# Kernel tuning notes

Hardware: AMD Instinct MI355X
Metric: run time of the kernel (lower is better)

The kernel has to match this reference:

```python
import jax, jax.numpy as jnp
import numpy as np

D_MODEL = 1024
NUM_HEADS = 16
HEAD_DIM = D_MODEL // NUM_HEADS

def setup_inputs() -> dict:
    key = jax.random.key(0)
    ks = jax.random.split(key, 9)
    B, L = 2, 2048
    s = 1.0 / np.sqrt(D_MODEL)
    return {
        "x":  jax.random.normal(ks[0], (B, L, D_MODEL), dtype=jnp.float32),
        "Wq": jax.random.uniform(ks[1], (D_MODEL, D_MODEL), jnp.float32, -s, s),
        "bq": jax.random.uniform(ks[2], (D_MODEL,), jnp.float32, -s, s),
        "Wk": jax.random.uniform(ks[3], (D_MODEL, D_MODEL), jnp.float32, -s, s),
        "bk": jax.random.uniform(ks[4], (D_MODEL,), jnp.float32, -s, s),
        "Wv": jax.random.uniform(ks[5], (D_MODEL, D_MODEL), jnp.float32, -s, s),
        "bv": jax.random.uniform(ks[6], (D_MODEL,), jnp.float32, -s, s),
        "Wo": jax.random.uniform(ks[7], (D_MODEL, D_MODEL), jnp.float32, -s, s),
        "bo": jax.random.uniform(ks[8], (D_MODEL,), jnp.float32, -s, s),
    }

def _split_heads(t):
    B, L, _ = t.shape
    return t.reshape(B, L, NUM_HEADS, HEAD_DIM).transpose(0, 2, 1, 3)  # [B,H,L,Dh]

def reference(x, Wq, bq, Wk, bk, Wv, bv, Wo, bo):
    # Linear projections (torch Linear: y = x @ W.T + b)
    Q = _split_heads(x @ Wq.T + bq)
    K = _split_heads(x @ Wk.T + bk)
    V = _split_heads(x @ Wv.T + bv)
    scale = 1.0 / jnp.sqrt(jnp.asarray(HEAD_DIM, dtype=x.dtype))
    scores = jnp.einsum('bhqd,bhkd->bhqk', Q, K) * scale  # [B,H,L,L]
    attn_weights = jax.nn.softmax(scores, axis=-1)
    ctx = jnp.einsum('bhqk,bhkd->bhqd', attn_weights, V)  # [B,H,L,Dh]
    B, H, L, Dh = ctx.shape
    ctx = ctx.transpose(0, 2, 1, 3).reshape(B, L, H * Dh)
    out = ctx @ Wo.T + bo  # dropout p=0.0 -> identity
    return (out, attn_weights)
```

## Files before the change

### kernel.cpp

```cpp
#include <hip/hip_runtime.h>

typedef unsigned short u16;
typedef __bf16 bf16x8 __attribute__((ext_vector_type(8)));
typedef float f32x4 __attribute__((ext_vector_type(4)));

#define WSTR 72
#define TSZ (64 * WSTR)

__device__ __forceinline__ u16 f2bf(float f) {
    union { float f; unsigned int u; } v; v.f = f;
    unsigned int u = v.u;
    u += 0x7fffu + ((u >> 16) & 1u);
    return (u16)(u >> 16);
}

__device__ __forceinline__ u16 cvt_bf(float f) {
    __bf16 h = (__bf16)f;
    union { __bf16 h; u16 u; } v; v.h = h; return v.u;
}

__device__ __forceinline__ void gload16(const u16* g, u16* l) {
    __builtin_amdgcn_global_load_lds((const __attribute__((address_space(1))) unsigned int*)(const void*)g,
                                     (__attribute__((address_space(3))) unsigned int*)(void*)l, 16, 0, 0);
}

#define MFMA16(A, B, C) __builtin_amdgcn_mfma_f32_16x16x32_bf16(A, B, C, 0, 0, 0)

__global__ __launch_bounds__(256) void k_cvtX(const float* __restrict__ src, u16* __restrict__ dst) {
    const size_t i = ((size_t)blockIdx.x * 256 + threadIdx.x) * 8;
    float4 v0 = *(const float4*)(src + i);
    float4 v1 = *(const float4*)(src + i + 4);
    u16 o[8];
    o[0] = f2bf(v0.x); o[1] = f2bf(v0.y); o[2] = f2bf(v0.z); o[3] = f2bf(v0.w);
    o[4] = f2bf(v1.x); o[5] = f2bf(v1.y); o[6] = f2bf(v1.z); o[7] = f2bf(v1.w);
    *(uint4*)(dst + i) = *(const uint4*)o;
}

__global__ __launch_bounds__(256) void k_cvtW(const float* __restrict__ w0, const float* __restrict__ w1,
                                              const float* __restrict__ w2, const float* __restrict__ w3,
                                              u16* __restrict__ dst) {
    const int z = blockIdx.z;
    const float* src = z == 0 ? w0 : z == 1 ? w1 : z == 2 ? w2 : w3;
    const size_t i = ((size_t)blockIdx.x * 256 + threadIdx.x) * 8;
    float4 v0 = *(const float4*)(src + i);
    float4 v1 = *(const float4*)(src + i + 4);
    u16 o[8];
    o[0] = f2bf(v0.x); o[1] = f2bf(v0.y); o[2] = f2bf(v0.z); o[3] = f2bf(v0.w);
    o[4] = f2bf(v1.x); o[5] = f2bf(v1.y); o[6] = f2bf(v1.z); o[7] = f2bf(v1.w);
    *(uint4*)(dst + (size_t)z * 1048576 + i) = *(const uint4*)o;
}

__global__ __launch_bounds__(256) void k_qkv(const u16* __restrict__ Xb, const u16* __restrict__ Wb,
                                             const float* __restrict__ bq, const float* __restrict__ bk,
                                             const float* __restrict__ bv,
                                             u16* __restrict__ Q, u16* __restrict__ Kd, u16* __restrict__ Vtmp) {
    __shared__ __align__(16) u16 lA[128 * 32];
    __shared__ __align__(16) u16 lB[128 * 32];
    const int t = threadIdx.x;
    const int n0 = blockIdx.x * 128;
    const int m0 = blockIdx.y * 128;
    const int lane = t & 63, wave = t >> 6;
    const int wm = (wave >> 1) * 64, wn = (wave & 1) * 64;
    const int quad = lane >> 4, m16 = lane & 15;
    const int r4 = t >> 2, c8 = (t & 3) * 8;
    f32x4 acc[4][4] = {};
    for (int k0 = 0; k0 < 1024; k0 += 32) {
        gload16(Xb + (size_t)(m0 + r4) * 1024 + k0 + c8,       &lA[t * 8]);
        gload16(Xb + (size_t)(m0 + 64 + r4) * 1024 + k0 + c8,  &lA[2048 + t * 8]);
        gload16(Wb + (size_t)(n0 + r4) * 1024 + k0 + c8,       &lB[t * 8]);
        gload16(Wb + (size_t)(n0 + 64 + r4) * 1024 + k0 + c8,  &lB[2048 + t * 8]);
        __syncthreads();
        bf16x8 af[4], bfr[4];
#pragma unroll
        for (int i = 0; i < 4; ++i) {
            af[i]  = *(const bf16x8*)(lA + (wm + i * 16 + m16) * 32 + quad * 8);
            bfr[i] = *(const bf16x8*)(lB + (wn + i * 16 + m16) * 32 + quad * 8);
        }
#pragma unroll
        for (int mi = 0; mi < 4; ++mi)
#pragma unroll
            for (int ni = 0; ni < 4; ++ni)
                acc[mi][ni] = MFMA16(af[mi], bfr[ni], acc[mi][ni]);
        __syncthreads();
    }
#pragma unroll
    for (int ni = 0; ni < 4; ++ni) {
        const int gcol = n0 + wn + ni * 16 + m16;
        const int mat = gcol >> 10;
        const int col = gcol & 1023;
        const int h = col >> 6, d = col & 63;
        const float bias = (mat == 0 ? bq : mat == 1 ? bk : bv)[col];
        u16* dst = mat == 0 ? Q : mat == 1 ? Kd : Vtmp;
#pragma unroll
        for (int mi = 0; mi < 4; ++mi)
#pragma unroll
            for (int e = 0; e < 4; ++e) {
                const int row = m0 + wm + mi * 16 + quad * 4 + e;
                const int b = row >> 11, l = row & 2047;
                dst[(((size_t)(b * 16 + h)) * 2048 + l) * 64 + d] = cvt_bf(acc[mi][ni][e] + bias);
            }
    }
}

__global__ __launch_bounds__(256) void k_vtr(const u16* __restrict__ Vtmp, u16* __restrict__ Vt) {
    __shared__ __align__(16) u16 ld[64 * WSTR];
    const int t = threadIdx.x;
    const int bh = blockIdx.y;
    const int l0 = blockIdx.x * 64;
    const int r = t >> 3, c8 = (t & 7) * 8;
    const u16* src = Vtmp + (size_t)bh * 2048 * 64 + (size_t)l0 * 64;
    *(uint4*)&ld[r * WSTR + c8]        = *(const uint4*)(src + (size_t)r * 64 + c8);
    *(uint4*)&ld[(r + 32) * WSTR + c8] = *(const uint4*)(src + (size_t)(r + 32) * 64 + c8);
    __syncthreads();
    u16* dst = Vt + (size_t)bh * 64 * 2048 + l0;
#pragma unroll
    for (int half = 0; half < 2; ++half) {
        const int d = r + half * 32;
        u16 p[8];
#pragma unroll
        for (int i = 0; i < 8; ++i) p[i] = ld[(c8 + i) * WSTR + d];
        *(uint4*)(dst + (size_t)d * 2048 + c8) = *(const uint4*)p;
    }
}

__global__ __launch_bounds__(256) void k_attn(const u16* __restrict__ Q,
                                              const u16* __restrict__ K,
                                              const u16* __restrict__ Vt,
                                              float* __restrict__ attn,
                                              u16* __restrict__ ctx) {
    __shared__ __align__(16) u16 lK[2 * TSZ];
    __shared__ __align__(16) u16 lV[2 * TSZ];
    __shared__ __align__(16) u16 lW[2 * TSZ];
    __shared__ float sred[2][64];
    const int t = threadIdx.x;
    const int bh = blockIdx.x;
    const int m0 = blockIdx.y * 64;
    const int lane = t & 63, wave = t >> 6;
    const int wq = (wave & 1) * 32;
    const int wk = (wave >> 1) * 32;
    const int wm = (wave >> 1) * 32, wn = (wave & 1) * 32;
    const int quad = lane >> 4, m16 = lane & 15;
    const int sr = t >> 3, sc = (t & 7) * 8;
    const u16* Qh = Q + (size_t)bh * 2048 * 64;
    const u16* Kh = K + (size_t)bh * 2048 * 64;
    const u16* Vh = Vt + (size_t)bh * 64 * 2048;
    float* ah = attn + ((size_t)bh << 22) + (size_t)m0 * 2048;

    const float SC = 0.18033688011112042f;

    bf16x8 qf[2][2];
#pragma unroll
    for (int ni = 0; ni < 2; ++ni)
#pragma unroll
        for (int ks = 0; ks < 2; ++ks)
            qf[ni][ks] = *(const bf16x8*)(Qh + (size_t)(m0 + wq + ni * 16 + m16) * 64 + ks * 32 + quad * 8);

    float slane[2] = {0.f, 0.f};
    {
        *(uint4*)&lK[sr * WSTR + sc]        = *(const uint4*)(Kh + (size_t)sr * 64 + sc);
        *(uint4*)&lK[(sr + 32) * WSTR + sc] = *(const uint4*)(Kh + (size_t)(sr + 32) * 64 + sc);
        int buf = 0;
        for (int kt = 0; kt < 32; ++kt) {
            __syncthreads();
            if (kt < 31) {
                const u16* kp = Kh + (size_t)(kt + 1) * 64 * 64;
                u16* dK = &lK[(buf ^ 1) * TSZ];
                *(uint4*)&dK[sr * WSTR + sc]        = *(const uint4*)(kp + (size_t)sr * 64 + sc);
                *(uint4*)&dK[(sr + 32) * WSTR + sc] = *(const uint4*)(kp + (size_t)(sr + 32) * 64 + sc);
            }
            const u16* lKb = &lK[buf * TSZ];
            bf16x8 k00 = *(const bf16x8*)(lKb + (wk + m16) * WSTR + quad * 8);
            bf16x8 k01 = *(const bf16x8*)(lKb + (wk + m16) * WSTR + 32 + quad * 8);
            bf16x8 k10 = *(const bf16x8*)(lKb + (wk + 16 + m16) * WSTR + quad * 8);
            bf16x8 k11 = *(const bf16x8*)(lKb + (wk + 16 + m16) * WSTR + 32 + quad * 8);
            f32x4 sacc[2][2] = {};
            sacc[0][0] = MFMA16(k00, qf[0][0], sacc[0][0]);
            sacc[0][1] = MFMA16(k00, qf[1][0], sacc[0][1]);
            sacc[1][0] = MFMA16(k10, qf[0][0], sacc[1][0]);
            sacc[1][1] = MFMA16(k10, qf[1][0], sacc[1][1]);
            sacc[0][0] = MFMA16(k01, qf[0][1], sacc[0][0]);
            sacc[0][1] = MFMA16(k01, qf[1][1], sacc[0][1]);
            sacc[1][0] = MFMA16(k11, qf[0][1], sacc[1][0]);
            sacc[1][1] = MFMA16(k11, qf[1][1], sacc[1][1]);
#pragma unroll
            for (int mi = 0; mi < 2; ++mi)
#pragma unroll
                for (int e = 0; e < 4; ++e) {
                    slane[0] += __builtin_amdgcn_exp2f(sacc[mi][0][e] * SC);
                    slane[1] += __builtin_amdgcn_exp2f(sacc[mi][1][e] * SC);
                }
            buf ^= 1;
        }
    }
#pragma unroll
    for (int ni = 0; ni < 2; ++ni) {
        slane[ni] += __shfl_xor(slane[ni], 16);
        slane[ni] += __shfl_xor(slane[ni], 32);
    }
    if (quad == 0) {
        sred[wave >> 1][wq + m16]      = slane[0];
        sred[wave >> 1][wq + 16 + m16] = slane[1];
    }
    __syncthreads();
    float inv[2];
    inv[0] = 1.0f / (sred[0][wq + m16]      + sred[1][wq + m16]);
    inv[1] = 1.0f / (sred[0][wq + 16 + m16] + sred[1][wq + 16 + m16]);

    unsigned aoff[2][2], lwoff[2][2];
#pragma unroll
    for (int mi = 0; mi < 2; ++mi)
#pragma unroll
        for (int ni = 0; ni < 2; ++ni) {
            const int q = wq + ni * 16 + m16;
            const int k = wk + mi * 16 + quad * 4;
            aoff[mi][ni]  = (unsigned)(q * 2048 + k);
            lwoff[mi][ni] = (unsigned)(q * WSTR + k);
        }

    f32x4 cacc[2][2] = {};
    bf16x8 vp00 = {}, vp01 = {}, vp10 = {}, vp11 = {};
    {
        *(uint4*)&lK[sr * WSTR + sc]        = *(const uint4*)(Kh + (size_t)sr * 64 + sc);
        *(uint4*)&lK[(sr + 32) * WSTR + sc] = *(const uint4*)(Kh + (size_t)(sr + 32) * 64 + sc);
        *(uint4*)&lV[sr * WSTR + sc]        = *(const uint4*)(Vh + (size_t)sr * 2048 + sc);
        *(uint4*)&lV[(sr + 32) * WSTR + sc] = *(const uint4*)(Vh + (size_t)(sr + 32) * 2048 + sc);
        int buf = 0;
        for (int kt = 0; kt < 32; ++kt) {
            __syncthreads();
            const u16* lKb = &lK[buf * TSZ];
            const u16* lVb = &lV[buf * TSZ];
            bf16x8 vn00 = *(const bf16x8*)(lVb + (wn + m16) * WSTR + quad * 8);
            bf16x8 vn01 = *(const bf16x8*)(lVb + (wn + m16) * WSTR + 32 + quad * 8);
            bf16x8 vn10 = *(const bf16x8*)(lVb + (wn + 16 + m16) * WSTR + quad * 8);
            bf16x8 vn11 = *(const bf16x8*)(lVb + (wn + 16 + m16) * WSTR + 32 + quad * 8);
            bf16x8 k00 = *(const bf16x8*)(lKb + (wk + m16) * WSTR + quad * 8);
            bf16x8 k01 = *(const bf16x8*)(lKb + (wk + m16) * WSTR + 32 + quad * 8);
            bf16x8 k10 = *(const bf16x8*)(lKb + (wk + 16 + m16) * WSTR + quad * 8);
            bf16x8 k11 = *(const bf16x8*)(lKb + (wk + 16 + m16) * WSTR + 32 + quad * 8);
            f32x4 sacc[2][2] = {};
            sacc[0][0] = MFMA16(k00, qf[0][0], sacc[0][0]);
            sacc[0][1] = MFMA16(k00, qf[1][0], sacc[0][1]);
            sacc[1][0] = MFMA16(k10, qf[0][0], sacc[1][0]);
            sacc[1][1] = MFMA16(k10, qf[1][0], sacc[1][1]);
            sacc[0][0] = MFMA16(k01, qf[0][1], sacc[0][0]);
            sacc[0][1] = MFMA16(k01, qf[1][1], sacc[0][1]);
            sacc[1][0] = MFMA16(k11, qf[0][1], sacc[1][0]);
            sacc[1][1] = MFMA16(k11, qf[1][1], sacc[1][1]);
            if (kt < 31) {
                const u16* kp = Kh + (size_t)(kt + 1) * 64 * 64;
                const u16* vp = Vh + (size_t)(kt + 1) * 64;
                u16* dK = &lK[(buf ^ 1) * TSZ];
                u16* dV = &lV[(buf ^ 1) * TSZ];
                *(uint4*)&dK[sr * WSTR + sc]        = *(const uint4*)(kp + (size_t)sr * 64 + sc);
                *(uint4*)&dK[(sr + 32) * WSTR + sc] = *(const uint4*)(kp + (size_t)(sr + 32) * 64 + sc);
                *(uint4*)&dV[sr * WSTR + sc]        = *(const uint4*)(vp + (size_t)sr * 2048 + sc);
                *(uint4*)&dV[(sr + 32) * WSTR + sc] = *(const uint4*)(vp + (size_t)(sr + 32) * 2048 + sc);
            }
#pragma unroll
            for (int mi = 0; mi < 2; ++mi)
#pragma unroll
                for (int ni = 0; ni < 2; ++ni)
#pragma unroll
                    for (int e = 0; e < 4; ++e)
                        sacc[mi][ni][e] = __builtin_amdgcn_exp2f(sacc[mi][ni][e] * SC) * inv[ni];
            u16* lwb = &lW[(kt & 1) * TSZ];
#pragma unroll
            for (int mi = 0; mi < 2; ++mi)
#pragma unroll
                for (int ni = 0; ni < 2; ++ni) {
                    u16 p[4];
                    p[0] = cvt_bf(sacc[mi][ni][0]); p[1] = cvt_bf(sacc[mi][ni][1]);
                    p[2] = cvt_bf(sacc[mi][ni][2]); p[3] = cvt_bf(sacc[mi][ni][3]);
                    *(uint2*)&lwb[lwoff[mi][ni]] = *(const uint2*)p;
                }
            float* ap = ah + kt * 64;
#pragma unroll
            for (int mi = 0; mi < 2; ++mi)
#pragma unroll
                for (int ni = 0; ni < 2; ++ni)
                    *(f32x4*)(ap + aoff[mi][ni]) = sacc[mi][ni];
            if (kt > 0) {
                const u16* lwp = &lW[((kt - 1) & 1) * TSZ];
                bf16x8 a00 = *(const bf16x8*)(lwp + (wm + m16) * WSTR + quad * 8);
                bf16x8 a01 = *(const bf16x8*)(lwp + (wm + m16) * WSTR + 32 + quad * 8);
                bf16x8 a10 = *(const bf16x8*)(lwp + (wm + 16 + m16) * WSTR + quad * 8);
                bf16x8 a11 = *(const bf16x8*)(lwp + (wm + 16 + m16) * WSTR + 32 + quad * 8);
                cacc[0][0] = MFMA16(a00, vp00, cacc[0][0]);
                cacc[0][1] = MFMA16(a00, vp10, cacc[0][1]);
                cacc[1][0] = MFMA16(a10, vp00, cacc[1][0]);
                cacc[1][1] = MFMA16(a10, vp10, cacc[1][1]);
                cacc[0][0] = MFMA16(a01, vp01, cacc[0][0]);
                cacc[0][1] = MFMA16(a01, vp11, cacc[0][1]);
                cacc[1][0] = MFMA16(a11, vp01, cacc[1][0]);
                cacc[1][1] = MFMA16(a11, vp11, cacc[1][1]);
            }
            vp00 = vn00; vp01 = vn01; vp10 = vn10; vp11 = vn11;
            buf ^= 1;
        }
        __syncthreads();
        const u16* lwp = &lW[(31 & 1) * TSZ];
        bf16x8 a00 = *(const bf16x8*)(lwp + (wm + m16) * WSTR + quad * 8);
        bf16x8 a01 = *(const bf16x8*)(lwp + (wm + m16) * WSTR + 32 + quad * 8);
        bf16x8 a10 = *(const bf16x8*)(lwp + (wm + 16 + m16) * WSTR + quad * 8);
        bf16x8 a11 = *(const bf16x8*)(lwp + (wm + 16 + m16) * WSTR + 32 + quad * 8);
        cacc[0][0] = MFMA16(a00, vp00, cacc[0][0]);
        cacc[0][1] = MFMA16(a00, vp10, cacc[0][1]);
        cacc[1][0] = MFMA16(a10, vp00, cacc[1][0]);
        cacc[1][1] = MFMA16(a10, vp10, cacc[1][1]);
        cacc[0][0] = MFMA16(a01, vp01, cacc[0][0]);
        cacc[0][1] = MFMA16(a01, vp11, cacc[0][1]);
        cacc[1][0] = MFMA16(a11, vp01, cacc[1][0]);
        cacc[1][1] = MFMA16(a11, vp11, cacc[1][1]);
    }

    const int b = bh >> 4, h = bh & 15;
    u16* cp = ctx + ((size_t)b * 2048) * 1024 + h * 64;
#pragma unroll
    for (int mi = 0; mi < 2; ++mi)
#pragma unroll
        for (int ni = 0; ni < 2; ++ni)
#pragma unroll
            for (int e = 0; e < 4; ++e) {
                const int row = m0 + wm + mi * 16 + quad * 4 + e;
                const int col = wn + ni * 16 + m16;
                cp[(size_t)row * 1024 + col] = cvt_bf(cacc[mi][ni][e]);
            }
}

__global__ __launch_bounds__(256) void k_out(const u16* __restrict__ ctx,
                                             const u16* __restrict__ WoB,
                                             const float* __restrict__ bo,
                                             float* __restrict__ out) {
    __shared__ __align__(16) u16 lA[128 * 32];
    __shared__ __align__(16) u16 lB[128 * 32];
    const int t = threadIdx.x;
    const int n0 = blockIdx.x * 128;
    const int m0 = blockIdx.y * 128;
    const int lane = t & 63, wave = t >> 6;
    const int wm = (wave >> 1) * 64, wn = (wave & 1) * 64;
    const int quad = lane >> 4, m16 = lane & 15;
    const int r4 = t >> 2, c8 = (t & 3) * 8;
    f32x4 acc[4][4] = {};
    for (int k0 = 0; k0 < 1024; k0 += 32) {
        gload16(ctx + (size_t)(m0 + r4) * 1024 + k0 + c8,       &lA[t * 8]);
        gload16(ctx + (size_t)(m0 + 64 + r4) * 1024 + k0 + c8,  &lA[2048 + t * 8]);
        gload16(WoB + (size_t)(n0 + r4) * 1024 + k0 + c8,       &lB[t * 8]);
        gload16(WoB + (size_t)(n0 + 64 + r4) * 1024 + k0 + c8,  &lB[2048 + t * 8]);
        __syncthreads();
        bf16x8 af[4], bfr[4];
#pragma unroll
        for (int i = 0; i < 4; ++i) {
            af[i]  = *(const bf16x8*)(lA + (wm + i * 16 + m16) * 32 + quad * 8);
            bfr[i] = *(const bf16x8*)(lB + (wn + i * 16 + m16) * 32 + quad * 8);
        }
#pragma unroll
        for (int mi = 0; mi < 4; ++mi)
#pragma unroll
            for (int ni = 0; ni < 4; ++ni)
                acc[mi][ni] = MFMA16(af[mi], bfr[ni], acc[mi][ni]);
        __syncthreads();
    }
#pragma unroll
    for (int ni = 0; ni < 4; ++ni) {
        const int col = n0 + wn + ni * 16 + m16;
        const float bv = bo[col];
#pragma unroll
        for (int mi = 0; mi < 4; ++mi)
#pragma unroll
            for (int e = 0; e < 4; ++e) {
                const int row = m0 + wm + mi * 16 + quad * 4 + e;
                out[(size_t)row * 1024 + col] = acc[mi][ni][e] + bv;
            }
    }
}

extern "C" void kernel_launch(void* const* d_in, const int* in_sizes, int n_in,
                              void* d_out, int out_size, void* d_ws, size_t ws_size,
                              hipStream_t stream) {
    const float* x  = (const float*)d_in[0];
    const float* Wq = (const float*)d_in[1];
    const float* bq = (const float*)d_in[2];
    const float* Wk = (const float*)d_in[3];
    const float* bk = (const float*)d_in[4];
    const float* Wv = (const float*)d_in[5];
    const float* bv = (const float*)d_in[6];
    const float* Wo = (const float*)d_in[7];
    const float* bo = (const float*)d_in[8];

    float* out_f = (float*)d_out;
    float* attn  = out_f + (size_t)4096 * 1024;

    u16* Xb = (u16*)d_ws;
    u16* Wb = Xb + (size_t)4194304;
    u16* Qb = Wb + (size_t)4194304;
    u16* Kb = Qb + (size_t)4194304;
    u16* Vt = Kb + (size_t)4194304;
    u16* Vtmp = (u16*)attn;

    dim3 blk(256);
    k_cvtX<<<dim3(2048), blk, 0, stream>>>(x, Xb);
    k_cvtW<<<dim3(512, 1, 4), blk, 0, stream>>>(Wq, Wk, Wv, Wo, Wb);
    k_qkv<<<dim3(24, 32), blk, 0, stream>>>(Xb, Wb, bq, bk, bv, Qb, Kb, Vtmp);
    k_vtr<<<dim3(32, 32), blk, 0, stream>>>(Vtmp, Vt);
    k_attn<<<dim3(32, 32), blk, 0, stream>>>(Qb, Kb, Vt, attn, Xb);
    k_out<<<dim3(8, 32), blk, 0, stream>>>(Xb, Wb + (size_t)3072 * 1024, bo, out_f);
}
```

Baseline: 703.0 us.

## Enlarge attention query tile to 128 rows per block for K/V reuse

Each attention block now handles 128 query rows instead of 64, and each wave covers 64 query rows with four Q fragments, so every K and V tile loaded into shared memory serves twice as many queries. The PV product's wave mapping is reorganised to match, and the grid is halved. The aim is to cut K/V global and LDS traffic per unit of work. In exchange the block uses more registers and a larger probability buffer in shared memory, and only 512 blocks are launched, which may lower occupancy.

Result: slower. 774.2 us (+10.1%).

```diff
diff --git a/kernel.cpp b/kernel.cpp
--- a/kernel.cpp
+++ b/kernel.cpp
@@ -6,6 +6,7 @@
 
 #define WSTR 72
 #define TSZ (64 * WSTR)
+#define WTSZ (128 * WSTR)
 
 __device__ __forceinline__ u16 f2bf(float f) {
     union { float f; unsigned int u; } v; v.f = f;
@@ -130,15 +131,14 @@
                                               u16* __restrict__ ctx) {
     __shared__ __align__(16) u16 lK[2 * TSZ];
     __shared__ __align__(16) u16 lV[2 * TSZ];
-    __shared__ __align__(16) u16 lW[2 * TSZ];
-    __shared__ float sred[2][64];
+    __shared__ __align__(16) u16 lW[2 * WTSZ];
+    __shared__ float sred[2][128];
     const int t = threadIdx.x;
     const int bh = blockIdx.x;
-    const int m0 = blockIdx.y * 64;
+    const int m0 = blockIdx.y * 128;
     const int lane = t & 63, wave = t >> 6;
-    const int wq = (wave & 1) * 32;
+    const int wq = (wave & 1) * 64;
     const int wk = (wave >> 1) * 32;
-    const int wm = (wave >> 1) * 32, wn = (wave & 1) * 32;
     const int quad = lane >> 4, m16 = lane & 15;
     const int sr = t >> 3, sc = (t & 7) * 8;
     const u16* Qh = Q + (size_t)bh * 2048 * 64;
@@ -148,14 +148,14 @@
 
     const float SC = 0.18033688011112042f;
 
-    bf16x8 qf[2][2];
-#pragma unroll
-    for (int ni = 0; ni < 2; ++ni)
+    bf16x8 qf[4][2];
+#pragma unroll
+    for (int ni = 0; ni < 4; ++ni)
 #pragma unroll
         for (int ks = 0; ks < 2; ++ks)
             qf[ni][ks] = *(const bf16x8*)(Qh + (size_t)(m0 + wq + ni * 16 + m16) * 64 + ks * 32 + quad * 8);
 
-    float slane[2] = {0.f, 0.f};
+    float slane[4] = {0.f, 0.f, 0.f, 0.f};
     {
         *(uint4*)&lK[sr * WSTR + sc]        = *(const uint4*)(Kh + (size_t)sr * 64 + sc);
         *(uint4*)&lK[(sr + 32) * WSTR + sc] = *(const uint4*)(Kh + (size_t)(sr + 32) * 64 + sc);
@@ -169,56 +169,58 @@
                 *(uint4*)&dK[(sr + 32) * WSTR + sc] = *(const uint4*)(kp + (size_t)(sr + 32) * 64 + sc);
             }
             const u16* lKb = &lK[buf * TSZ];
-            bf16x8 k00 = *(const bf16x8*)(lKb + (wk + m16) * WSTR + quad * 8);
-            bf16x8 k01 = *(const bf16x8*)(lKb + (wk + m16) * WSTR + 32 + quad * 8);
-            bf16x8 k10 = *(const bf16x8*)(lKb + (wk + 16 + m16) * WSTR + quad * 8);
-            bf16x8 k11 = *(const bf16x8*)(lKb + (wk + 16 + m16) * WSTR + 32 + quad * 8);
-            f32x4 sacc[2][2] = {};
-            sacc[0][0] = MFMA16(k00, qf[0][0], sacc[0][0]);
-            sacc[0][1] = MFMA16(k00, qf[1][0], sacc[0][1]);
-            sacc[1][0] = MFMA16(k10, qf[0][0], sacc[1][0]);
-            sacc[1][1] = MFMA16(k10, qf[1][0], sacc[1][1]);
-            sacc[0][0] = MFMA16(k01, qf[0][1], sacc[0][0]);
-            sacc[0][1] = MFMA16(k01, qf[1][1], sacc[0][1]);
-            sacc[1][0] = MFMA16(k11, qf[0][1], sacc[1][0]);
-            sacc[1][1] = MFMA16(k11, qf[1][1], sacc[1][1]);
-#pragma unroll
-            for (int mi = 0; mi < 2; ++mi)
-#pragma unroll
-                for (int e = 0; e < 4; ++e) {
-                    slane[0] += __builtin_amdgcn_exp2f(sacc[mi][0][e] * SC);
-                    slane[1] += __builtin_amdgcn_exp2f(sacc[mi][1][e] * SC);
+            f32x4 sacc[2][4] = {};
+#pragma unroll
+            for (int ks = 0; ks < 2; ++ks) {
+                bf16x8 k0 = *(const bf16x8*)(lKb + (wk + m16) * WSTR + ks * 32 + quad * 8);
+                bf16x8 k1 = *(const bf16x8*)(lKb + (wk + 16 + m16) * WSTR + ks * 32 + quad * 8);
+#pragma unroll
+                for (int ni = 0; ni < 4; ++ni) {
+                    sacc[0][ni] = MFMA16(k0, qf[ni][ks], sacc[0][ni]);
+                    sacc[1][ni] = MFMA16(k1, qf[ni][ks], sacc[1][ni]);
                 }
+            }
+#pragma unroll
+            for (int ni = 0; ni < 4; ++ni)
+#pragma unroll
+                for (int mi = 0; mi < 2; ++mi)
+#pragma unroll
+                    for (int e = 0; e < 4; ++e)
+                        slane[ni] += __builtin_amdgcn_exp2f(sacc[mi][ni][e] * SC);
             buf ^= 1;
         }
     }
 #pragma unroll
-    for (int ni = 0; ni < 2; ++ni) {
+    for (int ni = 0; ni < 4; ++ni) {
         slane[ni] += __shfl_xor(slane[ni], 16);
         slane[ni] += __shfl_xor(slane[ni], 32);
     }
     if (quad == 0) {
-        sred[wave >> 1][wq + m16]      = slane[0];
-        sred[wave >> 1][wq + 16 + m16] = slane[1];
+#pragma unroll
+        for (int ni = 0; ni < 4; ++ni)
+            sred[wave >> 1][wq + ni * 16 + m16] = slane[ni];
     }
     __syncthreads();
-    float inv[2];
-    inv[0] = 1.0f / (sred[0][wq + m16]      + sred[1][wq + m16]);
-    inv[1] = 1.0f / (sred[0][wq + 16 + m16] + sred[1][wq + 16 + m16]);
-
-    unsigned aoff[2][2], lwoff[2][2];
+    float inv[4];
+#pragma unroll
+    for (int ni = 0; ni < 4; ++ni) {
+        const int q = wq + ni * 16 + m16;
+        inv[ni] = 1.0f / (sred[0][q] + sred[1][q]);
+    }
+
+    unsigned aoff[2][4], lwoff[2][4];
 #pragma unroll
     for (int mi = 0; mi < 2; ++mi)
 #pragma unroll
-        for (int ni = 0; ni < 2; ++ni) {
+        for (int ni = 0; ni < 4; ++ni) {
             const int q = wq + ni * 16 + m16;
             const int k = wk + mi * 16 + quad * 4;
             aoff[mi][ni]  = (unsigned)(q * 2048 + k);
             lwoff[mi][ni] = (unsigned)(q * WSTR + k);
         }
 
-    f32x4 cacc[2][2] = {};
-    bf16x8 vp00 = {}, vp01 = {}, vp10 = {}, vp11 = {};
+    f32x4 cacc[4][2] = {};
+    bf16x8 vp[2][2] = {};
     {
         *(uint4*)&lK[sr * WSTR + sc]        = *(const uint4*)(Kh + (size_t)sr * 64 + sc);
         *(uint4*)&lK[(sr + 32) * WSTR + sc] = *(const uint4*)(Kh + (size_t)(sr + 32) * 64 + sc);
@@ -229,45 +231,45 @@
             __syncthreads();
             const u16* lKb = &lK[buf * TSZ];
             const u16* lVb = &lV[buf * TSZ];
-            bf16x8 vn00 = *(const bf16x8*)(lVb + (wn + m16) * WSTR + quad * 8);
-            bf16x8 vn01 = *(const bf16x8*)(lVb + (wn + m16) * WSTR + 32 + quad * 8);
-            bf16x8 vn10 = *(const bf16x8*)(lVb + (wn + 16 + m16) * WSTR + quad * 8);
-            bf16x8 vn11 = *(const bf16x8*)(lVb + (wn + 16 + m16) * WSTR + 32 + quad * 8);
-            bf16x8 k00 = *(const bf16x8*)(lKb + (wk + m16) * WSTR + quad * 8);
-            bf16x8 k01 = *(const bf16x8*)(lKb + (wk + m16) * WSTR + 32 + quad * 8);
-            bf16x8 k10 = *(const bf16x8*)(lKb + (wk + 16 + m16) * WSTR + quad * 8);
-            bf16x8 k11 = *(const bf16x8*)(lKb + (wk + 16 + m16) * WSTR + 32 + quad * 8);
-            f32x4 sacc[2][2] = {};
-            sacc[0][0] = MFMA16(k00, qf[0][0], sacc[0][0]);
-            sacc[0][1] = MFMA16(k00, qf[1][0], sacc[0][1]);
-            sacc[1][0] = MFMA16(k10, qf[0][0], sacc[1][0]);
-            sacc[1][1] = MFMA16(k10, qf[1][0], sacc[1][1]);
-            sacc[0][0] = MFMA16(k01, qf[0][1], sacc[0][0]);
-            sacc[0][1] = MFMA16(k01, qf[1][1], sacc[0][1]);
-            sacc[1][0] = MFMA16(k11, qf[0][1], sacc[1][0]);
-            sacc[1][1] = MFMA16(k11, qf[1][1], sacc[1][1]);
+            bf16x8 vn[2][2];
+#pragma unroll
+            for (int nj = 0; nj < 2; ++nj)
+#pragma unroll
+                for (int ks = 0; ks < 2; ++ks)
+                    vn[nj][ks] = *(const bf16x8*)(lVb + (wk + nj * 16 + m16) * WSTR + ks * 32 + quad * 8);
+            f32x4 sacc[2][4] = {};
+#pragma unroll
+            for (int ks = 0; ks < 2; ++ks) {
+                bf16x8 k0 = *(const bf16x8*)(lKb + (wk + m16) * WSTR + ks * 32 + quad * 8);
+                bf16x8 k1 = *(const bf16x8*)(lKb + (wk + 16 + m16) * WSTR + ks * 32 + quad * 8);
+#pragma unroll
+                for (int ni = 0; ni < 4; ++ni) {
+                    sacc[0][ni] = MFMA16(k0, qf[ni][ks], sacc[0][ni]);
+                    sacc[1][ni] = MFMA16(k1, qf[ni][ks], sacc[1][ni]);
+                }
+            }
             if (kt < 31) {
                 const u16* kp = Kh + (size_t)(kt + 1) * 64 * 64;
-                const u16* vp = Vh + (size_t)(kt + 1) * 64;
+                const u16* vp2 = Vh + (size_t)(kt + 1) * 64;
                 u16* dK = &lK[(buf ^ 1) * TSZ];
                 u16* dV = &lV[(buf ^ 1) * TSZ];
                 *(uint4*)&dK[sr * WSTR + sc]        = *(const uint4*)(kp + (size_t)sr * 64 + sc);
                 *(uint4*)&dK[(sr + 32) * WSTR + sc] = *(const uint4*)(kp + (size_t)(sr + 32) * 64 + sc);
-                *(uint4*)&dV[sr * WSTR + sc]        = *(const uint4*)(vp + (size_t)sr * 2048 + sc);
-                *(uint4*)&dV[(sr + 32) * WSTR + sc] = *(const uint4*)(vp + (size_t)(sr + 32) * 2048 + sc);
+                *(uint4*)&dV[sr * WSTR + sc]        = *(const uint4*)(vp2 + (size_t)sr * 2048 + sc);
+                *(uint4*)&dV[(sr + 32) * WSTR + sc] = *(const uint4*)(vp2 + (size_t)(sr + 32) * 2048 + sc);
             }
 #pragma unroll
             for (int mi = 0; mi < 2; ++mi)
 #pragma unroll
-                for (int ni = 0; ni < 2; ++ni)
+                for (int ni = 0; ni < 4; ++ni)
 #pragma unroll
                     for (int e = 0; e < 4; ++e)
                         sacc[mi][ni][e] = __builtin_amdgcn_exp2f(sacc[mi][ni][e] * SC) * inv[ni];
-            u16* lwb = &lW[(kt & 1) * TSZ];
+            u16* lwb = &lW[(kt & 1) * WTSZ];
 #pragma unroll
             for (int mi = 0; mi < 2; ++mi)
 #pragma unroll
-                for (int ni = 0; ni < 2; ++ni) {
+                for (int ni = 0; ni < 4; ++ni) {
                     u16 p[4];
                     p[0] = cvt_bf(sacc[mi][ni][0]); p[1] = cvt_bf(sacc[mi][ni][1]);
                     p[2] = cvt_bf(sacc[mi][ni][2]); p[3] = cvt_bf(sacc[mi][ni][3]);
@@ -277,53 +279,49 @@
 #pragma unroll
             for (int mi = 0; mi < 2; ++mi)
 #pragma unroll
-                for (int ni = 0; ni < 2; ++ni)
+                for (int ni = 0; ni < 4; ++ni)
                     *(f32x4*)(ap + aoff[mi][ni]) = sacc[mi][ni];
             if (kt > 0) {
-                const u16* lwp = &lW[((kt - 1) & 1) * TSZ];
-                bf16x8 a00 = *(const bf16x8*)(lwp + (wm + m16) * WSTR + quad * 8);
-                bf16x8 a01 = *(const bf16x8*)(lwp + (wm + m16) * WSTR + 32 + quad * 8);
-                bf16x8 a10 = *(const bf16x8*)(lwp + (wm + 16 + m16) * WSTR + quad * 8);
-                bf16x8 a11 = *(const bf16x8*)(lwp + (wm + 16 + m16) * WSTR + 32 + quad * 8);
-                cacc[0][0] = MFMA16(a00, vp00, cacc[0][0]);
-                cacc[0][1] = MFMA16(a00, vp10, cacc[0][1]);
-                cacc[1][0] = MFMA16(a10, vp00, cacc[1][0]);
-                cacc[1][1] = MFMA16(a10, vp10, cacc[1][1]);
-                cacc[0][0] = MFMA16(a01, vp01, cacc[0][0]);
-                cacc[0][1] = MFMA16(a01, vp11, cacc[0][1]);
-                cacc[1][0] = MFMA16(a11, vp01, cacc[1][0]);
-                cacc[1][1] = MFMA16(a11, vp11, cacc[1][1]);
-            }
-            vp00 = vn00; vp01 = vn01; vp10 = vn10; vp11 = vn11;
+                const u16* lwp = &lW[((kt - 1) & 1) * WTSZ];
+#pragma unroll
+                for (int ks = 0; ks < 2; ++ks)
+#pragma unroll
+                    for (int mi = 0; mi < 4; ++mi) {
+                        bf16x8 a = *(const bf16x8*)(lwp + (wq + mi * 16 + m16) * WSTR + ks * 32 + quad * 8);
+                        cacc[mi][0] = MFMA16(a, vp[0][ks], cacc[mi][0]);
+                        cacc[mi][1] = MFMA16(a, vp[1][ks], cacc[mi][1]);
+                    }
+            }
+#pragma unroll
+            for (int nj = 0; nj < 2; ++nj)
+#pragma unroll
+                for (int ks = 0; ks < 2; ++ks)
+                    vp[nj][ks] = vn[nj][ks];
             buf ^= 1;
         }
         __syncthreads();
-        const u16* lwp = &lW[(31 & 1) * TSZ];
-        bf16x8 a00 = *(const bf16x8*)(lwp + (wm + m16) * WSTR + quad * 8);
-        bf16x8 a01 = *(const bf16x8*)(lwp + (wm + m16) * WSTR + 32 + quad * 8);
-        bf16x8 a10 = *(const bf16x8*)(lwp + (wm + 16 + m16) * WSTR + quad * 8);
-        bf16x8 a11 = *(const bf16x8*)(lwp + (wm + 16 + m16) * WSTR + 32 + quad * 8);
-        cacc[0][0] = MFMA16(a00, vp00, cacc[0][0]);
-        cacc[0][1] = MFMA16(a00, vp10, cacc[0][1]);
-        cacc[1][0] = MFMA16(a10, vp00, cacc[1][0]);
-        cacc[1][1] = MFMA16(a10, vp10, cacc[1][1]);
-        cacc[0][0] = MFMA16(a01, vp01, cacc[0][0]);
-        cacc[0][1] = MFMA16(a01, vp11, cacc[0][1]);
-        cacc[1][0] = MFMA16(a11, vp01, cacc[1][0]);
-        cacc[1][1] = MFMA16(a11, vp11, cacc[1][1]);
+        const u16* lwp = &lW[(31 & 1) * WTSZ];
+#pragma unroll
+        for (int ks = 0; ks < 2; ++ks)
+#pragma unroll
+            for (int mi = 0; mi < 4; ++mi) {
+                bf16x8 a = *(const bf16x8*)(lwp + (wq + mi * 16 + m16) * WSTR + ks * 32 + quad * 8);
+                cacc[mi][0] = MFMA16(a, vp[0][ks], cacc[mi][0]);
+                cacc[mi][1] = MFMA16(a, vp[1][ks], cacc[mi][1]);
+            }
     }
 
     const int b = bh >> 4, h = bh & 15;
     u16* cp = ctx + ((size_t)b * 2048) * 1024 + h * 64;
 #pragma unroll
-    for (int mi = 0; mi < 2; ++mi)
-#pragma unroll
-        for (int ni = 0; ni < 2; ++ni)
+    for (int mi = 0; mi < 4; ++mi)
+#pragma unroll
+        for (int nj = 0; nj < 2; ++nj)
 #pragma unroll
             for (int e = 0; e < 4; ++e) {
-                const int row = m0 + wm + mi * 16 + quad * 4 + e;
-                const int col = wn + ni * 16 + m16;
-                cp[(size_t)row * 1024 + col] = cvt_bf(cacc[mi][ni][e]);
+                const int row = m0 + wq + mi * 16 + quad * 4 + e;
+                const int col = wk + nj * 16 + m16;
+                cp[(size_t)row * 1024 + col] = cvt_bf(cacc[mi][nj][e]);
             }
 }
 
@@ -402,6 +400,6 @@
     k_cvtW<<<dim3(512, 1, 4), blk, 0, stream>>>(Wq, Wk, Wv, Wo, Wb);
     k_qkv<<<dim3(24, 32), blk, 0, stream>>>(Xb, Wb, bq, bk, bv, Qb, Kb, Vtmp);
     k_vtr<<<dim3(32, 32), blk, 0, stream>>>(Vtmp, Vt);
-    k_attn<<<dim3(32, 32), blk, 0, stream>>>(Qb, Kb, Vt, attn, Xb);
+    k_attn<<<dim3(32, 16), blk, 0, stream>>>(Qb, Kb, Vt, attn, Xb);
     k_out<<<dim3(8, 32), blk, 0, stream>>>(Xb, Wb + (size_t)3072 * 1024, bo, out_f);
 }
```
